# Optimization experiments

Measured on AMD Instinct MI355X. Metric: run time of the kernel, lower is better.

## Reference

```python
import jax, jax.numpy as jnp
import numpy as np

# dims matching init_kwargs
L, D, NH = 4, 1024, 16          # num_blocks, embed_dim, num_heads
HD = D // NH                     # head dim
CUR, MEM, BS, IN = 512, 512, 8, 512
FF = 4 * D
GRU_BIAS = 2.0

def sinusoidal_pe(full_seq, dim):
    # SinusoidalPE: freqs = arange(0, dim, 2); inv = 10000**(-freqs/dim); seq descending
    freqs = jnp.arange(0, dim, 2.0)
    inv = 10000.0 ** (-freqs / dim)
    seq = jnp.arange(full_seq - 1, -1, -1.0)
    ang = seq[:, None] * inv[None, :]                       # (full, dim/2)
    return jnp.concatenate([jnp.sin(ang), jnp.cos(ang)], axis=-1)  # (full, dim)

def layer_norm(x, g, b, eps=1e-5):
    m = x.mean(-1, keepdims=True)
    v = ((x - m) ** 2).mean(-1, keepdims=True)
    return (x - m) * jax.lax.rsqrt(v + eps) * g + b

def rel_shift(x):
    # Transformer-XL relative shift. x: (q, k, b, h)
    q, k, b, h = x.shape
    zp = jnp.zeros((q, 1, b, h), x.dtype)
    return jnp.concatenate([zp, x], axis=1).reshape(k + 1, q, b, h)[1:].reshape(q, k, b, h)

def gru_gate(x, y, W):
    # W: (6, D, D) = Wr, Ur, Wz, Uz, Wg, Ug (no bias except learned-ish gru_bias on z)
    Wr, Ur, Wz, Uz, Wg, Ug = W[0], W[1], W[2], W[3], W[4], W[5]
    r = jax.nn.sigmoid(y @ Wr.T + x @ Ur.T)
    z = jax.nn.sigmoid(y @ Wz.T + x @ Uz.T - GRU_BIAS)
    hh = jnp.tanh(y @ Wg.T + (r * x) @ Ug.T)
    return (1.0 - z) * x + z * hh

def rel_attn(q, k, v, pos, U, V, mask, W):
    # q: (cur, bs, D); k, v: (full, bs, D); pos: (full, D); W: (5, D, D) = Wq,Wk,Wv,Wr,Wo
    cur, bs, _ = q.shape
    full = k.shape[0]
    qh = (q @ W[0].T).reshape(cur, bs, NH, HD)
    kh = (k @ W[1].T).reshape(full, bs, NH, HD)
    vh = (v @ W[2].T).reshape(full, bs, NH, HD)
    rh = (pos @ W[3].T).reshape(full, NH, HD)
    AC = jnp.einsum('ibhd,jbhd->ijbh', qh + U, kh)          # content stream with U bias
    BD = rel_shift(jnp.einsum('ibhd,jhd->ijbh', qh + V, rh))  # position stream with V bias
    score = (AC + BD) * (1.0 / np.sqrt(HD))
    score = jnp.where(mask[:, :, None, None], jnp.asarray(-1e30, score.dtype), score)
    attn = jax.nn.softmax(score, axis=1)
    out = jnp.einsum('ijbh,jbhd->ibhd', attn, vh).reshape(cur, bs, D)
    return out @ W[4].T

def gelu(x):
    return jax.nn.gelu(x, approximate=False)  # torch nn.GELU default is exact

def _forward(h, memory, W_emb, b_emb, U, V, ln1, ln2, Wattn, g1, g2, fc_W1, fc_b1, fc_W2, fc_b2):
    h = jnp.transpose(h, (1, 0, 2))            # (cur, bs, in)
    mem = jax.lax.stop_gradient(memory)        # memory holds detached hidden states
    cur = h.shape[0]
    prev = mem.shape[1]
    full = cur + prev
    x = gelu(h @ W_emb.T + b_emb)              # linear embedding + GELU activation
    pos = sinusoidal_pe(full, D)               # (full, D); pos_emb.unsqueeze(1) broadcast over bs
    mask = jnp.triu(jnp.ones((cur, full), bool), 1 + prev)
    out = x
    for i in range(L):
        key = jnp.concatenate([mem[i], out], axis=0)   # (full, bs, D)
        nq = layer_norm(out, ln1[i, 0], ln1[i, 1])
        nk = layer_norm(key, ln1[i, 0], ln1[i, 1])
        Y = rel_attn(nq, nk, nk, pos, U, V, mask, Wattn[i])
        Y = gelu(Y)                                     # dropout is identity (eval / p=0)
        o1 = gru_gate(out, Y, g1[i])
        E = layer_norm(o1, ln2[i, 0], ln2[i, 1])
        E = gelu(gelu(E @ fc_W1[i].T + fc_b1[i]) @ fc_W2[i].T + fc_b2[i])
        out = gru_gate(o1, E, g2[i])
    return jnp.transpose(out, (1, 0, 2))       # (bs, cur, D)

def setup_inputs() -> dict:
    key = jax.random.key(0)
    ks = jax.random.split(key, 12)
    s = 0.02
    eye2 = jnp.stack([jnp.ones(D, jnp.float32), jnp.zeros(D, jnp.float32)])  # (gamma, beta)
    return {
        'h': jax.random.normal(ks[0], (BS, CUR, IN), jnp.float32),
        'memory': jax.random.normal(ks[1], (L, MEM, BS, D), jnp.float32),
        'W_emb': jax.random.normal(ks[2], (D, IN), jnp.float32) * s,
        'b_emb': jnp.zeros((D,), jnp.float32),
        'U': jax.random.normal(ks[3], (NH, HD), jnp.float32) * s,
        'V': jax.random.normal(ks[4], (NH, HD), jnp.float32) * s,
        'ln1': jnp.tile(eye2[None], (L, 1, 1)),
        'ln2': jnp.tile(eye2[None], (L, 1, 1)),
        'Wattn': jax.random.normal(ks[5], (L, 5, D, D), jnp.float32) * s,  # q,k,v,r,o per block
        'g1': jax.random.normal(ks[6], (L, 6, D, D), jnp.float32) * s,
        'g2': jax.random.normal(ks[7], (L, 6, D, D), jnp.float32) * s,
        'fc_W1': jax.random.normal(ks[8], (L, FF, D), jnp.float32) * s,
        'fc_b1': jnp.zeros((L, FF), jnp.float32),
        'fc_W2': jax.random.normal(ks[9], (L, D, FF), jnp.float32) * s,
        'fc_b2': jnp.zeros((L, D), jnp.float32),
    }

def reference(h, memory, W_emb, b_emb, U, V, ln1, ln2, Wattn, g1, g2, fc_W1, fc_b1, fc_W2, fc_b2):
    return _forward(h, memory, W_emb, b_emb, U, V, ln1, ln2, Wattn, g1, g2, fc_W1, fc_b1, fc_W2, fc_b2)
```

## Files before the change

kernel.cpp:

```cpp
#include <hip/hip_runtime.h>
#include <hip/hip_bf16.h>


typedef __attribute__((ext_vector_type(8))) __bf16 bfrag;
typedef __attribute__((ext_vector_type(4))) float f4;
typedef __attribute__((ext_vector_type(4))) unsigned short u16x4;
typedef __attribute__((ext_vector_type(8))) unsigned short u16x8;

__device__ __forceinline__ unsigned short f2bf(float f){
  union { float f; unsigned u; } v; v.f = f;
  unsigned r = v.u + 0x7fffu + ((v.u >> 16) & 1u);
  return (unsigned short)(r >> 16);
}
__device__ __forceinline__ float bf2f(unsigned short u){
  union { unsigned u; float f; } v; v.u = (unsigned)u << 16; return v.f;
}
__device__ __forceinline__ float geluf(float x){
  return 0.5f * x * (1.0f + erff(x * 0.7071067811865476f));
}
__device__ __forceinline__ float sigm(float x){ return 1.0f/(1.0f + __expf(-x)); }

__device__ __forceinline__ void gl_lds(const void* g, void* l){
  __builtin_amdgcn_global_load_lds(
    reinterpret_cast<const __attribute__((address_space(1))) unsigned int*>(
        reinterpret_cast<unsigned long>(g)),
    reinterpret_cast<__attribute__((address_space(3))) unsigned int*>(
        reinterpret_cast<unsigned long>(l)),
    16, 0, 0);
}

struct GP {
  const unsigned short* A;
  const unsigned short* A2;
  const unsigned short* B;
  const unsigned short* B2;
  unsigned short* O1;
  unsigned short* O2;
  unsigned short* O3;
  unsigned short* O4;
  unsigned short* O5;
  float* OF;
  const float* bias1;
  const float* bias2;
  const float* X;
  const float* Z;
  int K, Ksplit, lda, ldb, ldo;
  int sBz;
};

template<int BM, int BN, int EPI>
__global__ __launch_bounds__(256) void gemm_k(GP p){
  __shared__ unsigned short As[BM*32];
  __shared__ unsigned short Bs[BN*32];
  const int tid  = threadIdx.x;
  const int lane = tid & 63;
  const int wid  = tid >> 6;
  const int lr   = lane & 15;
  const int lg   = lane >> 4;
  constexpr int FM = BM/32, FN = BN/32;
  const int m0 = blockIdx.y * BM;
  const int n0 = blockIdx.x * BN;
  const int z  = blockIdx.z;

  const unsigned short* Abase = p.A;
  const unsigned short* Bbase = p.B;
  if constexpr (EPI==13){
    if (z==2){ if (blockIdx.y >= 32) return; Abase = p.A + 4194304; }
    if (z==3){ if (blockIdx.y >= 8)  return; Abase = p.A2; }
    const int zsel = (z==0)?1:((z==1)?2:((z==2)?0:3));
    Bbase = p.B + (long)zsel*1048576;
  }

  const int ksp = p.Ksplit ? p.Ksplit : p.K;
  const unsigned short* AbL = Abase + (long)m0*p.lda;
  const unsigned short* AbH = p.A2 && EPI!=13 ? (p.A2 + (long)m0*p.lda - ksp) : AbL;
  const unsigned short* BbL = Bbase + (long)z*p.sBz + (long)n0*p.ldb;
  const unsigned short* BbH = p.B2 ? (p.B2 + (long)z*p.sBz + (long)n0*p.ldb - ksp) : BbL;

  const int srow = tid >> 2;
  const int skk  = (tid & 3) * 8;

  f4 acc[FM][FN];
  f4 zero4 = {0.0f, 0.0f, 0.0f, 0.0f};
  #pragma unroll
  for (int m=0;m<FM;m++)
    #pragma unroll
    for (int n=0;n<FN;n++) acc[m][n] = zero4;

  for (int k0 = 0; k0 < p.K; k0 += 32){
    const unsigned short* A_ = (k0 < ksp) ? AbL : AbH;
    const unsigned short* B_ = (k0 < ksp) ? BbL : BbH;
    #pragma unroll
    for (int q=0;q<BM/64;q++)
      gl_lds(A_ + (long)(q*64 + srow)*p.lda + k0 + skk, (char*)As + q*4096 + wid*1024);
    #pragma unroll
    for (int q=0;q<BN/64;q++)
      gl_lds(B_ + (long)(q*64 + srow)*p.ldb + k0 + skk, (char*)Bs + q*4096 + wid*1024);
    __syncthreads();
    bfrag af[FM], bfr[FN];
    #pragma unroll
    for (int m=0;m<FM;m++)
      af[m] = *(const bfrag*)&As[((wid>>1)*(BM/2) + m*16 + lr)*32 + lg*8];
    #pragma unroll
    for (int n=0;n<FN;n++)
      bfr[n] = *(const bfrag*)&Bs[((wid&1)*(BN/2) + n*16 + lr)*32 + lg*8];
    #pragma unroll
    for (int m=0;m<FM;m++)
      #pragma unroll
      for (int n=0;n<FN;n++)
        acc[m][n] = __builtin_amdgcn_mfma_f32_16x16x32_bf16(af[m], bfr[n], acc[m][n], 0, 0, 0);
    __syncthreads();
  }

  const int wr0 = m0 + (wid>>1)*(BM/2);
  const int wc0 = n0 + (wid&1)*(BN/2);
  #pragma unroll
  for (int m=0;m<FM;m++)
    #pragma unroll
    for (int n=0;n<FN;n++)
      #pragma unroll
      for (int r=0;r<4;r++){
        const int gr = wr0 + m*16 + lg*4 + r;
        const int gc = wc0 + n*16 + lr;
        const float a = acc[m][n][r];
        const long base = (long)gr*p.ldo + gc;
        if constexpr (EPI==6){
          const float t = a + (p.bias1 ? p.bias1[gc] : 0.0f);
          p.O1[base] = f2bf(geluf(t));
        }
        else if constexpr (EPI==7){
          const float t = geluf(a + p.bias1[gc]);
          p.OF[base] = t; p.O1[base] = f2bf(t);
        }
        else if constexpr (EPI==11){
          const long ix = (long)gr*1024 + gc;
          if (z==0) p.O1[ix] = f2bf(sigm(a) * p.X[ix]);
          else      p.OF[ix] = sigm(a - 2.0f);
        }
        else if constexpr (EPI==12){
          const long ix = (long)gr*1024 + gc;
          const float zz = p.Z[ix];
          const float oo = (1.0f - zz)*p.X[ix] + zz*tanhf(a);
          p.OF[ix] = oo; p.O1[ix] = f2bf(oo);
        }
        else if constexpr (EPI==13){
          const long ix = (long)gr*1024 + gc;
          if (z==0){ p.O1[ix] = f2bf(a); }
          else if (z==1){
            const int b_ = gr & 7, js = gr >> 3, h_ = gc >> 6, d_ = gc & 63;
            p.O2[(long)(b_*16 + h_)*65536 + (long)d_*1024 + js] = f2bf(a);
          }
          else if (z==2){ p.O3[ix] = f2bf((a + p.bias1[gc])*0.125f);
                          p.O4[ix] = f2bf((a + p.bias2[gc])*0.125f); }
          else { p.O5[ix] = f2bf(a); }
        }
      }
}

__global__ __launch_bounds__(256,3) void attn_k(const unsigned short* __restrict__ qU,
                                                const unsigned short* __restrict__ qV,
                                                const unsigned short* __restrict__ kh,
                                                const unsigned short* __restrict__ rh,
                                                const unsigned short* __restrict__ vhT,
                                                unsigned short* __restrict__ ctx){
  __shared__ char Sm[20480];
  __shared__ float redm[4][16];
  __shared__ float reds[4][16];
  __shared__ float invd[16];
  const int tid = threadIdx.x;
  const int w   = tid >> 6;
  const int lane= tid & 63;
  const int lr  = lane & 15;
  const int lg  = lane >> 4;
  const int id = blockIdx.x;
  const int b  = id & 7;
  const int i0 = ((id >> 3) & 31) * 16;
  const int h  = id >> 8;
  const long hoff = (long)h * 64;
  const f4 z4 = {0.f,0.f,0.f,0.f};

  bfrag bqv[2];
  #pragma unroll
  for (int kk=0;kk<2;kk++)
    bqv[kk] = *(const bfrag*)(qV + ((long)(i0 + lr)*8 + b)*1024 + hoff + kk*32 + lg*8);
  bfrag aq[2];
  #pragma unroll
  for (int kk=0;kk<2;kk++)
    aq[kk] = *(const bfrag*)(qU + ((long)(i0 + lr)*8 + b)*1024 + hoff + kk*32 + lg*8);

  f4 s[16];

  #pragma unroll
  for (int half=0; half<2; ++half){
    const int c0    = half*512;
    const int rbase = half ? (1008 - i0) : (496 - i0);
    const int ntil  = half ? (1 + (i0>>4)) : 33;
    const int radd  = half ? -497 : 15;
    for (int mt = w; mt < ntil; mt += 4){
      const int r0 = rbase + mt*16;
      f4 acc = z4;
      #pragma unroll
      for (int kk=0;kk<2;kk++){
        bfrag ar = *(const bfrag*)(rh + (long)(r0 + lr)*1024 + hoff + kk*32 + lg*8);
        acc = __builtin_amdgcn_mfma_f32_16x16x32_bf16(ar, bqv[kk], acc, 0,0,0);
      }
      #pragma unroll
      for (int q=0;q<4;q++){
        const int rr = mt*16 + lg*4 + q;
        *(unsigned short*)(Sm + rr*32 + ((lr*2) ^ ((rr&15)<<1))) = f2bf(acc[q]);
      }
    }
    __syncthreads();
    const int cw = c0 + w*128;
    #pragma unroll
    for (int n=0;n<8;n++){
      f4 a = z4;
      #pragma unroll
      for (int kk=0;kk<2;kk++){
        bfrag bk = *(const bfrag*)(kh + ((long)(cw + n*16 + lr)*8 + b)*1024 + hoff + kk*32 + lg*8);
        a = __builtin_amdgcn_mfma_f32_16x16x32_bf16(aq[kk], bk, a, 0,0,0);
      }
      #pragma unroll
      for (int q=0;q<4;q++){
        const int di = lg*4 + q;
        const int jc = cw + n*16 + lr;
        if (jc > i0 + di + 512) a[q] = -1e30f;
        else {
          const int rr = jc - di + radd;
          a[q] += bf2f(*(const unsigned short*)(Sm + rr*32 + (((di*2)) ^ ((rr&15)<<1))));
        }
      }
      s[half*8 + n] = a;
    }
    __syncthreads();
  }

  float mx[4], sum[4];
  #pragma unroll
  for (int q=0;q<4;q++){
    float m = -3.0e38f;
    #pragma unroll
    for (int n=0;n<16;n++) m = fmaxf(m, fmaxf(fmaxf(s[n][q], s[n][q]), s[n][q]));
    m = s[0][q];
    #pragma unroll
    for (int n=1;n<16;n++) m = fmaxf(m, s[n][q]);
    m = fmaxf(m, __shfl_xor(m, 1));
    m = fmaxf(m, __shfl_xor(m, 2));
    m = fmaxf(m, __shfl_xor(m, 4));
    m = fmaxf(m, __shfl_xor(m, 8));
    if (lr == 0) redm[w][lg*4+q] = m;
  }
  __syncthreads();
  #pragma unroll
  for (int q=0;q<4;q++){
    const int row = lg*4+q;
    mx[q] = fmaxf(fmaxf(redm[0][row], redm[1][row]), fmaxf(redm[2][row], redm[3][row]));
    sum[q] = 0.0f;
  }
  #pragma unroll
  for (int n=0;n<16;n++)
    #pragma unroll
    for (int q=0;q<4;q++){
      const float e = __expf(s[n][q] - mx[q]);
      s[n][q] = e;
      sum[q] += e;
    }
  #pragma unroll
  for (int q=0;q<4;q++){
    float v = sum[q];
    v += __shfl_xor(v, 1);
    v += __shfl_xor(v, 2);
    v += __shfl_xor(v, 4);
    v += __shfl_xor(v, 8);
    if (lr == 0) reds[w][lg*4+q] = v;
  }
  __syncthreads();
  if (tid < 16)
    invd[tid] = 1.0f / (reds[0][tid] + reds[1][tid] + reds[2][tid] + reds[3][tid]);

  f4 oac[4];
  #pragma unroll
  for (int nd=0;nd<4;nd++) oac[nd] = z4;
  const unsigned short* vb_base = vhT + (long)(b*16 + h)*65536;
  char* Pch = Sm + w*1024;
  #pragma unroll
  for (int t=0;t<8;t++){
    const int jb = (t < 4) ? (w*128 + t*32) : (512 + w*128 + (t-4)*32);
    #pragma unroll
    for (int nn=0;nn<2;nn++){
      const f4 e = s[2*t + nn];
      #pragma unroll
      for (int q=0;q<4;q++){
        const int row = lg*4 + q;
        const int col = nn*16 + lr;
        *(unsigned short*)(Pch + row*64 + ((col*2) ^ (((row>>2)&3)<<4))) = f2bf(e[q]);
      }
    }
    bfrag pa = *(const bfrag*)(Pch + lr*64 + ((lg*16) ^ (((lr>>2)&3)<<4)));
    #pragma unroll
    for (int nd=0;nd<4;nd++){
      bfrag bv = *(const bfrag*)(vb_base + (long)(nd*16 + lr)*1024 + jb + lg*8);
      oac[nd] = __builtin_amdgcn_mfma_f32_16x16x32_bf16(pa, bv, oac[nd], 0,0,0);
    }
  }
  float* po = (float*)(Sm + 4096 + w*4096);
  #pragma unroll
  for (int nd=0;nd<4;nd++)
    #pragma unroll
    for (int q=0;q<4;q++)
      po[(lg*4+q)*64 + nd*16 + lr] = oac[nd][q];
  __syncthreads();
  {
    const int row = tid >> 4;
    const int d0  = (tid & 15) * 4;
    f4 v = *(const f4*)(Sm + 4096 + (row*64 + d0)*4);
    #pragma unroll
    for (int ww=1;ww<4;ww++){
      const f4 u = *(const f4*)(Sm + 4096 + ww*4096 + (row*64 + d0)*4);
      v.x += u.x; v.y += u.y; v.z += u.z; v.w += u.w;
    }
    const float iv = invd[row];
    u16x4 o;
    o.x = f2bf(v.x*iv); o.y = f2bf(v.y*iv); o.z = f2bf(v.z*iv); o.w = f2bf(v.w*iv);
    *(u16x4*)(ctx + ((long)(i0 + row)*8 + b)*1024 + hoff + d0) = o;
  }
}

__global__ __launch_bounds__(256) void ln_k(const float* __restrict__ srcA,
                                            const float* __restrict__ srcB, int splitRow,
                                            const float* __restrict__ g, const float* __restrict__ b,
                                            unsigned short* __restrict__ dst){
  const int row = blockIdx.x;
  const float* src = (srcB != nullptr && row >= splitRow)
                       ? (srcB + (long)(row - splitRow)*1024)
                       : (srcA + (long)row*1024);
  const int t = threadIdx.x;
  float4 v = ((const float4*)src)[t];
  float s1 = v.x+v.y+v.z+v.w;
  float s2 = v.x*v.x+v.y*v.y+v.z*v.z+v.w*v.w;
  #pragma unroll
  for (int o=32;o;o>>=1){ s1 += __shfl_xor(s1,o); s2 += __shfl_xor(s2,o); }
  __shared__ float r1[4], r2[4];
  const int w = t>>6;
  if ((t&63)==0){ r1[w]=s1; r2[w]=s2; }
  __syncthreads();
  s1 = r1[0]+r1[1]+r1[2]+r1[3];
  s2 = r2[0]+r2[1]+r2[2]+r2[3];
  const float mean = s1*(1.0f/1024.0f);
  const float var  = s2*(1.0f/1024.0f) - mean*mean;
  const float rs   = rsqrtf(var + 1e-5f);
  float4 gg = ((const float4*)g)[t];
  float4 bb = ((const float4*)b)[t];
  u16x4 o;
  o.x = f2bf((v.x-mean)*rs*gg.x + bb.x);
  o.y = f2bf((v.y-mean)*rs*gg.y + bb.y);
  o.z = f2bf((v.z-mean)*rs*gg.z + bb.z);
  o.w = f2bf((v.w-mean)*rs*gg.w + bb.w);
  *(u16x4*)(dst + (long)row*1024 + t*4) = o;
}

__global__ __launch_bounds__(256) void conv_k(const float* __restrict__ s,
                                              unsigned short* __restrict__ d, long n){
  long i = ((long)blockIdx.x*256 + threadIdx.x)*4;
  if (i >= n) return;
  float4 v = *(const float4*)(s + i);
  u16x4 o; o.x=f2bf(v.x); o.y=f2bf(v.y); o.z=f2bf(v.z); o.w=f2bf(v.w);
  *(u16x4*)(d + i) = o;
}

__global__ __launch_bounds__(128) void ht_k(const float* __restrict__ h,
                                            unsigned short* __restrict__ d){
  const int row = blockIdx.x;
  const int i = row>>3, b = row&7;
  const float* src = h + ((long)b*512 + i)*512;
  const int t = threadIdx.x;
  float4 v = ((const float4*)src)[t];
  u16x4 o; o.x=f2bf(v.x); o.y=f2bf(v.y); o.z=f2bf(v.z); o.w=f2bf(v.w);
  *(u16x4*)(d + (long)row*512 + t*4) = o;
}

__global__ __launch_bounds__(256) void pos_k(unsigned short* __restrict__ d){
  const int r = blockIdx.x, t = threadIdx.x;
  const float seq = (float)(1023 - r);
  u16x4 o;
  #pragma unroll
  for (int q=0;q<4;q++){
    const int c = t*4 + q;
    const int f = (c < 512) ? c : (c - 512);
    const float inv = expf((float)f * -0.017988946039016f);
    const float ang = seq * inv;
    const float val = (c < 512) ? sinf(ang) : cosf(ang);
    o[q] = f2bf(val);
  }
  *(u16x4*)(d + (long)r*1024 + t*4) = o;
}

__global__ __launch_bounds__(256) void outT_k(const float* __restrict__ o,
                                              float* __restrict__ d){
  const int row = blockIdx.x;
  const int b = row>>9, i = row&511;
  const float4 v = ((const float4*)(o + ((long)i*8 + b)*1024))[threadIdx.x];
  ((float4*)(d + (long)row*1024))[threadIdx.x] = v;
}

extern "C" void kernel_launch(void* const* d_in, const int* in_sizes, int n_in,
                              void* d_out, int out_size, void* d_ws, size_t ws_size,
                              hipStream_t stream){
  (void)in_sizes; (void)n_in; (void)out_size; (void)ws_size;
  const float* h     = (const float*)d_in[0];
  const float* memin = (const float*)d_in[1];
  const float* Wemb  = (const float*)d_in[2];
  const float* bemb  = (const float*)d_in[3];
  const float* Ub    = (const float*)d_in[4];
  const float* Vb    = (const float*)d_in[5];
  const float* ln1   = (const float*)d_in[6];
  const float* ln2   = (const float*)d_in[7];
  const float* Wattn = (const float*)d_in[8];
  const float* g1w   = (const float*)d_in[9];
  const float* g2w   = (const float*)d_in[10];
  const float* fw1   = (const float*)d_in[11];
  const float* fb1   = (const float*)d_in[12];
  const float* fw2   = (const float*)d_in[13];
  const float* fb2   = (const float*)d_in[14];

  char* Wp = (char*)d_ws;
  size_t off = 0;
  auto take = [&](size_t bytes)->size_t{ size_t r = off; off += (bytes + 255) & ~(size_t)255; return r; };
  float*          outf = (float*)         (Wp + take(16777216));
  unsigned short* xbf  = (unsigned short*)(Wp + take( 8388608));
  float*          o1f  = (float*)         (Wp + take(16777216));
  unsigned short* o1b  = (unsigned short*)(Wp + take( 8388608));
  float*          zbf  = (float*)         (Wp + take(16777216));
  unsigned short* rxb  = (unsigned short*)(Wp + take( 8388608));
  unsigned short* yb   = (unsigned short*)(Wp + take( 8388608));
  unsigned short* Eb   = (unsigned short*)(Wp + take( 8388608));
  unsigned short* wb0  = (unsigned short*)(Wp + take(52428800));
  unsigned short* hTb  = (unsigned short*)(Wp + take( 4194304));
  unsigned short* webb = (unsigned short*)(Wp + take( 1048576));
  unsigned short* posb = (unsigned short*)(Wp + take( 2097152));
  unsigned short* nkb  = (unsigned short*)(Wp + take(16777216));
  unsigned short* qUb  = (unsigned short*)(Wp + take( 8388608));
  unsigned short* qVb  = (unsigned short*)(Wp + take( 8388608));
  unsigned short* khb  = (unsigned short*)(Wp + take(16777216));
  unsigned short* vhTb = (unsigned short*)(Wp + take(16777216));
  unsigned short* F1b  = khb;
  unsigned short* rhb  = (unsigned short*)(Wp + take( 2097152));
  unsigned short* ctxb = (unsigned short*)(Wp + take( 8388608));

  const int M1 = 1048576;

  conv_k<<<512, 256, 0, stream>>>(Wemb, webb, 524288);
  ht_k<<<4096, 128, 0, stream>>>(h, hTb);
  pos_k<<<1024, 256, 0, stream>>>(posb);

  {
    GP p{}; p.A=hTb; p.B=webb; p.OF=outf; p.O1=xbf; p.bias1=bemb;
    p.K=512; p.lda=512; p.ldb=512; p.ldo=1024;
    gemm_k<128,64,7><<<dim3(16,32,1),256,0,stream>>>(p);
  }

  auto gru_fn = [&](const unsigned short* xb, const float* xf, const unsigned short* yb_,
                    const unsigned short* w6, float* of, unsigned short* ob){
    { GP p{}; p.A=yb_; p.A2=xb; p.B=w6; p.B2=w6+M1; p.sBz=2*M1;
      p.O1=rxb; p.OF=zbf; p.X=xf;
      p.K=2048; p.Ksplit=1024; p.lda=1024; p.ldb=1024; p.ldo=1024;
      gemm_k<128,128,11><<<dim3(8,32,2),256,0,stream>>>(p); }
    { GP p{}; p.A=yb_; p.A2=rxb; p.B=w6+4*M1; p.B2=w6+5*M1;
      p.X=xf; p.Z=zbf; p.OF=of; p.O1=ob;
      p.K=2048; p.Ksplit=1024; p.lda=1024; p.ldb=1024; p.ldo=1024;
      gemm_k<128,64,12><<<dim3(16,32,1),256,0,stream>>>(p); }
  };

  for (int l = 0; l < 4; ++l){
    conv_k<<<5120,256,0,stream>>>(Wattn + (long)l*5242880, wb0,          5242880);
    conv_k<<<6144,256,0,stream>>>(g1w   + (long)l*6291456, wb0 +  5*M1,  6291456);
    conv_k<<<6144,256,0,stream>>>(g2w   + (long)l*6291456, wb0 + 11*M1,  6291456);
    conv_k<<<4096,256,0,stream>>>(fw1   + (long)l*4194304, wb0 + 17*M1,  4194304);
    conv_k<<<4096,256,0,stream>>>(fw2   + (long)l*4194304, wb0 + 21*M1,  4194304);

    ln_k<<<8192,256,0,stream>>>(memin + (long)l*4194304, outf, 4096,
                                ln1 + l*2048, ln1 + l*2048 + 1024, nkb);

    {
      GP p{}; p.A=nkb; p.A2=posb; p.B=wb0;
      p.O1=khb; p.O2=vhTb; p.O3=qUb; p.O4=qVb; p.O5=rhb;
      p.bias1=Ub; p.bias2=Vb;
      p.K=1024; p.lda=1024; p.ldb=1024; p.ldo=1024;
      gemm_k<128,128,13><<<dim3(8,64,4),256,0,stream>>>(p); }

    attn_k<<<4096,256,0,stream>>>(qUb, qVb, khb, rhb, vhTb, ctxb);

    {
      GP p{}; p.A=ctxb; p.B=wb0+4*M1; p.O1=yb;
      p.K=1024; p.lda=1024; p.ldb=1024; p.ldo=1024;
      gemm_k<128,64,6><<<dim3(16,32,1),256,0,stream>>>(p); }

    gru_fn(xbf, outf, yb, wb0 + 5*M1, o1f, o1b);

    ln_k<<<4096,256,0,stream>>>(o1f, nullptr, 1<<30,
                                ln2 + l*2048, ln2 + l*2048 + 1024, Eb);

    { GP p{}; p.A=Eb;  p.B=wb0+17*M1; p.O1=F1b; p.bias1=fb1 + l*4096;
      p.K=1024; p.lda=1024; p.ldb=1024; p.ldo=4096;
      gemm_k<128,128,6><<<dim3(32,32,1),256,0,stream>>>(p); }
    { GP p{}; p.A=F1b; p.B=wb0+21*M1; p.O1=yb; p.bias1=fb2 + l*1024;
      p.K=4096; p.lda=4096; p.ldb=4096; p.ldo=1024;
      gemm_k<128,64,6><<<dim3(16,32,1),256,0,stream>>>(p); }

    gru_fn(o1b, o1f, yb, wb0 + 11*M1, outf, xbf);
  }

  outT_k<<<4096,256,0,stream>>>(outf, (float*)d_out);
}
```

Measured before the change: 3.083 ms.

## Double-buffer GEMM LDS tiles, retune attention occupancy and scratch layout

New measurement: 3.028 ms. About the same (-1.8%).

```diff
diff --git a/kernel.cpp b/kernel.cpp
--- a/kernel.cpp
+++ b/kernel.cpp
@@ -50,8 +50,8 @@
 
 template<int BM, int BN, int EPI>
 __global__ __launch_bounds__(256) void gemm_k(GP p){
-  __shared__ unsigned short As[BM*32];
-  __shared__ unsigned short Bs[BN*32];
+  __shared__ unsigned short As[2][BM*32];
+  __shared__ unsigned short Bs[2][BN*32];
   const int tid  = threadIdx.x;
   const int lane = tid & 63;
   const int wid  = tid >> 6;
@@ -87,29 +87,42 @@
     #pragma unroll
     for (int n=0;n<FN;n++) acc[m][n] = zero4;
 
-  for (int k0 = 0; k0 < p.K; k0 += 32){
-    const unsigned short* A_ = (k0 < ksp) ? AbL : AbH;
-    const unsigned short* B_ = (k0 < ksp) ? BbL : BbH;
-    #pragma unroll
-    for (int q=0;q<BM/64;q++)
-      gl_lds(A_ + (long)(q*64 + srow)*p.lda + k0 + skk, (char*)As + q*4096 + wid*1024);
-    #pragma unroll
-    for (int q=0;q<BN/64;q++)
-      gl_lds(B_ + (long)(q*64 + srow)*p.ldb + k0 + skk, (char*)Bs + q*4096 + wid*1024);
-    __syncthreads();
+  const int nk = p.K >> 5;
+  #pragma unroll
+  for (int q=0;q<BM/64;q++)
+    gl_lds(AbL + (long)(q*64 + srow)*p.lda + skk, (char*)As[0] + q*4096 + wid*1024);
+  #pragma unroll
+  for (int q=0;q<BN/64;q++)
+    gl_lds(BbL + (long)(q*64 + srow)*p.ldb + skk, (char*)Bs[0] + q*4096 + wid*1024);
+  __syncthreads();
+
+  int cur = 0;
+  for (int t = 0; t < nk; ++t){
+    const int k1 = (t+1) << 5;
+    if (t+1 < nk){
+      const unsigned short* A_ = (k1 < ksp) ? AbL : AbH;
+      const unsigned short* B_ = (k1 < ksp) ? BbL : BbH;
+      #pragma unroll
+      for (int q=0;q<BM/64;q++)
+        gl_lds(A_ + (long)(q*64 + srow)*p.lda + k1 + skk, (char*)As[cur^1] + q*4096 + wid*1024);
+      #pragma unroll
+      for (int q=0;q<BN/64;q++)
+        gl_lds(B_ + (long)(q*64 + srow)*p.ldb + k1 + skk, (char*)Bs[cur^1] + q*4096 + wid*1024);
+    }
     bfrag af[FM], bfr[FN];
     #pragma unroll
     for (int m=0;m<FM;m++)
-      af[m] = *(const bfrag*)&As[((wid>>1)*(BM/2) + m*16 + lr)*32 + lg*8];
+      af[m] = *(const bfrag*)&As[cur][((wid>>1)*(BM/2) + m*16 + lr)*32 + lg*8];
     #pragma unroll
     for (int n=0;n<FN;n++)
-      bfr[n] = *(const bfrag*)&Bs[((wid&1)*(BN/2) + n*16 + lr)*32 + lg*8];
+      bfr[n] = *(const bfrag*)&Bs[cur][((wid&1)*(BN/2) + n*16 + lr)*32 + lg*8];
     #pragma unroll
     for (int m=0;m<FM;m++)
       #pragma unroll
       for (int n=0;n<FN;n++)
         acc[m][n] = __builtin_amdgcn_mfma_f32_16x16x32_bf16(af[m], bfr[n], acc[m][n], 0, 0, 0);
     __syncthreads();
+    cur ^= 1;
   }
 
   const int wr0 = m0 + (wid>>1)*(BM/2);
@@ -157,7 +170,7 @@
       }
 }
 
-__global__ __launch_bounds__(256,3) void attn_k(const unsigned short* __restrict__ qU,
+__global__ __launch_bounds__(256,6) void attn_k(const unsigned short* __restrict__ qU,
                                                 const unsigned short* __restrict__ qV,
                                                 const unsigned short* __restrict__ kh,
                                                 const unsigned short* __restrict__ rh,
@@ -207,7 +220,7 @@
       #pragma unroll
       for (int q=0;q<4;q++){
         const int rr = mt*16 + lg*4 + q;
-        *(unsigned short*)(Sm + rr*32 + ((lr*2) ^ ((rr&15)<<1))) = f2bf(acc[q]);
+        *(unsigned short*)(Sm + rr*38 + lr*2) = f2bf(acc[q]);
       }
     }
     __syncthreads();
@@ -227,7 +240,7 @@
         if (jc > i0 + di + 512) a[q] = -1e30f;
         else {
           const int rr = jc - di + radd;
-          a[q] += bf2f(*(const unsigned short*)(Sm + rr*32 + (((di*2)) ^ ((rr&15)<<1))));
+          a[q] += bf2f(*(const unsigned short*)(Sm + rr*38 + di*2));
         }
       }
       s[half*8 + n] = a;
@@ -238,10 +251,7 @@
   float mx[4], sum[4];
   #pragma unroll
   for (int q=0;q<4;q++){
-    float m = -3.0e38f;
-    #pragma unroll
-    for (int n=0;n<16;n++) m = fmaxf(m, fmaxf(fmaxf(s[n][q], s[n][q]), s[n][q]));
-    m = s[0][q];
+    float m = s[0][q];
     #pragma unroll
     for (int n=1;n<16;n++) m = fmaxf(m, s[n][q]);
     m = fmaxf(m, __shfl_xor(m, 1));
@@ -288,7 +298,7 @@
     const int jb = (t < 4) ? (w*128 + t*32) : (512 + w*128 + (t-4)*32);
     #pragma unroll
     for (int nn=0;nn<2;nn++){
-      const f4 e = s[2*t + nn];
+      const f4 e = s[((t<4)?0:8) + (t&3)*2 + nn];
       #pragma unroll
       for (int q=0;q<4;q++){
         const int row = lg*4 + q;
@@ -464,7 +474,7 @@
     { GP p{}; p.A=yb_; p.A2=xb; p.B=w6; p.B2=w6+M1; p.sBz=2*M1;
       p.O1=rxb; p.OF=zbf; p.X=xf;
       p.K=2048; p.Ksplit=1024; p.lda=1024; p.ldb=1024; p.ldo=1024;
-      gemm_k<128,128,11><<<dim3(8,32,2),256,0,stream>>>(p); }
+      gemm_k<128,64,11><<<dim3(16,32,2),256,0,stream>>>(p); }
     { GP p{}; p.A=yb_; p.A2=rxb; p.B=w6+4*M1; p.B2=w6+5*M1;
       p.X=xf; p.Z=zbf; p.OF=of; p.O1=ob;
       p.K=2048; p.Ksplit=1024; p.lda=1024; p.ldb=1024; p.ldo=1024;
```
